# Optimization experiments

Measured on AMD Instinct MI355X. Metric: run time of the kernel, lower is better.

The kernel has to match this reference:

```python
import jax, jax.numpy as jnp
import numpy as np

B, M, NH, EH = 16, 128, 256, 128


def setup_inputs() -> dict:
    key = jax.random.key(0)
    ks = jax.random.split(key, 10)
    s = 0.05
    return {
        "X": jax.random.normal(ks[0], (B, M, NH), dtype=jnp.float32),
        "E": jax.random.normal(ks[1], (B, M, M, EH), dtype=jnp.float32),
        "A": jax.random.uniform(ks[2], (B, M, M), dtype=jnp.float32),
        "w": jax.random.uniform(ks[3], (B, M, 1), dtype=jnp.float32),
        "Wv_w": jax.random.normal(ks[4], (NH, NH), dtype=jnp.float32) * s,
        "Wv_b": jnp.zeros((NH,), dtype=jnp.float32),
        "We_w": jax.random.normal(ks[5], (EH, EH), dtype=jnp.float32) * s,
        "We_b": jnp.zeros((EH,), dtype=jnp.float32),
        "Wu_w": jax.random.normal(ks[6], (2 * NH + EH, NH), dtype=jnp.float32) * s,
        "Wu_b": jnp.zeros((NH,), dtype=jnp.float32),
    }


def reference(X, E, A, w, Wv_w, Wv_b, We_w, We_b, Wu_w, Wu_b):
    act = jax.nn.relu
    # W_v / W_e single-layer FFNs (capacity=0 -> one Linear)
    node_map = X @ Wv_w + Wv_b                      # [B, m, nh]
    edge_map = E @ We_w + We_b                      # [B, m, m, eh]
    # Fused aggregation: sum_i A[b,i,j] * cat(node_map[b,i], edge_map[b,i,j])
    # (avoids materializing the [B,m,m,nh+eh] intermediate; same math)
    agg_node = jnp.einsum('bij,bid->bjd', A, node_map)   # [B, m, nh]
    agg_edge = jnp.einsum('bij,bije->bje', A, edge_map)  # [B, m, eh]
    h = jnp.concatenate([agg_node, agg_edge, X], axis=2) # [B, m, 2nh+eh]
    out = (act(h) @ Wu_w + Wu_b) * w                     # [B, m, nh]
    return out
```

## Files before the change

### kernel.cpp

```cpp
#include <hip/hip_runtime.h>

namespace {

constexpr int Bn   = 16;
constexpr int Mn   = 128;
constexpr int NHn  = 256;
constexpr int EHn  = 128;
constexpr int ROWS = Bn * Mn;
constexpr int HW   = 2 * NHn + EHn;

constexpr int HP = HW + 4;
constexpr int AP = NHn + 4;
constexpr int TP = EHn + 4;

__device__ __forceinline__ float4 f4zero() { return make_float4(0.f, 0.f, 0.f, 0.f); }
__device__ __forceinline__ float4 ld4(const float* p) {
    return *reinterpret_cast<const float4*>(p);
}
__device__ __forceinline__ void f4fma(float4& acc, float a, const float4& v) {
    acc.x = fmaf(a, v.x, acc.x);
    acc.y = fmaf(a, v.y, acc.y);
    acc.z = fmaf(a, v.z, acc.z);
    acc.w = fmaf(a, v.w, acc.w);
}
__device__ __forceinline__ float4 f4add(const float4& a, const float4& b) {
    return make_float4(a.x + b.x, a.y + b.y, a.z + b.z, a.w + b.w);
}
__device__ __forceinline__ float4 f4relu(const float4& a) {
    return make_float4(fmaxf(a.x, 0.f), fmaxf(a.y, 0.f),
                       fmaxf(a.z, 0.f), fmaxf(a.w, 0.f));
}

#define LOADW(B, wb, ldw, kk) {                                        \
    const float* _wp = (wb) + (size_t)(kk) * (ldw);                    \
    B[0] = ld4(_wp);                 B[1] = ld4(_wp + (ldw));          \
    B[2] = ld4(_wp + 2 * (ldw));     B[3] = ld4(_wp + 3 * (ldw)); }

#define FMA2R(B, kk, opA, opB) {                                       \
    const float4 _ha = ld4(&(opA)[kk]);                                \
    const float4 _hb = ld4(&(opB)[kk]);                                \
    f4fma(a0, _ha.x, B[0]); f4fma(a1, _hb.x, B[0]);                    \
    f4fma(a0, _ha.y, B[1]); f4fma(a1, _hb.y, B[1]);                    \
    f4fma(a0, _ha.z, B[2]); f4fma(a1, _hb.z, B[2]);                    \
    f4fma(a0, _ha.w, B[3]); f4fma(a1, _hb.w, B[3]); }

#define FMA1R(B, kk, opA) {                                            \
    const float4 _ha = ld4(&(opA)[kk]);                                \
    f4fma(a0, _ha.x, B[0]); f4fma(a0, _ha.y, B[1]);                    \
    f4fma(a0, _ha.z, B[2]); f4fma(a0, _ha.w, B[3]); }

__global__ __launch_bounds__(256) void k_reduce(
    const float* __restrict__ E, const float* __restrict__ A,
    float* __restrict__ T)
{
    const int bid = blockIdx.x;
    const int b   = bid >> 5;
    const int j0  = (bid & 31) * 4;
    const int tid = threadIdx.x;

    __shared__ float acolT[4][Mn];

    if (tid < Mn) {
        const float4 a4 = ld4(A + (size_t)b * Mn * Mn + (size_t)tid * Mn + j0);
        acolT[0][tid] = a4.x; acolT[1][tid] = a4.y;
        acolT[2][tid] = a4.z; acolT[3][tid] = a4.w;
    }
    __syncthreads();

    const int jj = tid >> 6;
    const int f2 = tid & 63;
    const float* Eb = E + (size_t)b * Mn * Mn * EHn + (size_t)(j0 + jj) * EHn
                        + f2 * 2;
    const float* ac = acolT[jj];

    float2 acc = make_float2(0.f, 0.f);
    #pragma unroll 16
    for (int i = 0; i < Mn; ++i) {
        const float2 e2 = *reinterpret_cast<const float2*>(
            Eb + (size_t)i * (Mn * EHn));
        const float a = ac[i];
        acc.x = fmaf(a, e2.x, acc.x);
        acc.y = fmaf(a, e2.y, acc.y);
    }

    const int row = b * Mn + j0 + jj;
    *reinterpret_cast<float2*>(T + (size_t)row * EHn + f2 * 2) = acc;
}

__global__ __launch_bounds__(512, 2) void k_mix(
    const float* __restrict__ T, const float* __restrict__ A,
    const float* __restrict__ X,
    const float* __restrict__ Wv, const float* __restrict__ Wvb,
    const float* __restrict__ We, const float* __restrict__ Web,
    const float* __restrict__ Wu, const float* __restrict__ Wub,
    const float* __restrict__ wrow, float* __restrict__ out)
{
    const int r0  = blockIdx.x * 8;
    const int b   = r0 >> 7;
    const int j0  = r0 & 127;
    const int tid = threadIdx.x;

    __shared__ float  asl[Mn][8];
    __shared__ float  ts[8][TP];
    __shared__ float  axs[8][AP];
    __shared__ float  hs[8][HP];
    __shared__ float4 comb[256][2];
    __shared__ float  pcs[8][8];
    __shared__ float  csb[8];

    {
        const int i = tid >> 2, q = tid & 3;
        const float2 a2 = *reinterpret_cast<const float2*>(
            A + (size_t)b * Mn * Mn + (size_t)i * Mn + j0 + q * 2);
        asl[i][q * 2]     = a2.x;
        asl[i][q * 2 + 1] = a2.y;
    }
    if (tid < 256) {
        const int r = tid >> 5, c = tid & 31;
        *reinterpret_cast<float4*>(&ts[r][c * 4]) =
            ld4(T + (size_t)(r0 + r) * EHn + c * 4);
    }
    {
        const int r = tid >> 6, c4 = tid & 63;
        const float4 x4 = ld4(X + (size_t)(r0 + r) * NHn + c4 * 4);
        *reinterpret_cast<float4*>(&hs[r][NHn + EHn + c4 * 4]) = f4relu(x4);
    }
    __syncthreads();

    const int t8 = tid & 255;
    const int rg = t8 >> 6;
    const int c4 = t8 & 63;
    const int kh = tid >> 8;
    const int ra = 2 * rg, rb = ra + 1;

    if (tid < 64) {
        const int r = tid >> 3, seg = tid & 7;
        float s = 0.f;
        #pragma unroll
        for (int i = 0; i < 16; ++i) s += asl[seg * 16 + i][r];
        pcs[r][seg] = s;
    }

    {
        const float* wb = X + (size_t)(b * Mn) * NHn + c4 * 4;
        const int k0 = kh * 64;
        float4 B0[4], B1[4];
        float4 a0 = f4zero(), a1 = f4zero();
        LOADW(B0, wb, NHn, k0);
        for (int k = k0; k < k0 + 64; k += 8) {
            LOADW(B1, wb, NHn, k + 4);
            {
                const float4 _b = B0[0];
                (void)_b;
            }
            {
                f4fma(a0, asl[k    ][ra], B0[0]); f4fma(a1, asl[k    ][rb], B0[0]);
                f4fma(a0, asl[k + 1][ra], B0[1]); f4fma(a1, asl[k + 1][rb], B0[1]);
                f4fma(a0, asl[k + 2][ra], B0[2]); f4fma(a1, asl[k + 2][rb], B0[2]);
                f4fma(a0, asl[k + 3][ra], B0[3]); f4fma(a1, asl[k + 3][rb], B0[3]);
            }
            if (k + 8 < k0 + 64) LOADW(B0, wb, NHn, k + 8);
            {
                f4fma(a0, asl[k + 4][ra], B1[0]); f4fma(a1, asl[k + 4][rb], B1[0]);
                f4fma(a0, asl[k + 5][ra], B1[1]); f4fma(a1, asl[k + 5][rb], B1[1]);
                f4fma(a0, asl[k + 6][ra], B1[2]); f4fma(a1, asl[k + 6][rb], B1[2]);
                f4fma(a0, asl[k + 7][ra], B1[3]); f4fma(a1, asl[k + 7][rb], B1[3]);
            }
        }
        if (kh == 1) { comb[t8][0] = a0; comb[t8][1] = a1; }
        __syncthreads();
        if (kh == 0) {
            a0 = f4add(a0, comb[t8][0]);
            a1 = f4add(a1, comb[t8][1]);
            *reinterpret_cast<float4*>(&axs[ra][c4 * 4]) = a0;
            *reinterpret_cast<float4*>(&axs[rb][c4 * 4]) = a1;
        }
        if (tid < 8) {
            float s = 0.f;
            #pragma unroll
            for (int g = 0; g < 8; ++g) s += pcs[tid][g];
            csb[tid] = s;
        }
        __syncthreads();
    }

    if (tid < 256) {
        const int er = tid >> 5;
        const int ec = tid & 31;
        const float* wb = We + ec * 4;
        const float* opA = ts[er];
        float4 B0[4], B1[4];
        float4 a0 = f4zero();
        LOADW(B0, wb, EHn, 0);
        for (int k = 0; k < EHn; k += 8) {
            LOADW(B1, wb, EHn, k + 4);
            FMA1R(B0, k, opA);
            if (k + 8 < EHn) LOADW(B0, wb, EHn, k + 8);
            FMA1R(B1, k + 4, opA);
        }
        const float4 be = ld4(Web + ec * 4);
        f4fma(a0, csb[er], be);
        *reinterpret_cast<float4*>(&hs[er][NHn + ec * 4]) = f4relu(a0);
    }

    {
        const float* wb = Wv + c4 * 4;
        const float* opA = axs[ra];
        const float* opB = axs[rb];
        const int k0 = kh * 128;
        float4 B0[4], B1[4];
        float4 a0 = f4zero(), a1 = f4zero();
        LOADW(B0, wb, NHn, k0);
        for (int k = k0; k < k0 + 128; k += 8) {
            LOADW(B1, wb, NHn, k + 4);
            FMA2R(B0, k, opA, opB);
            if (k + 8 < k0 + 128) LOADW(B0, wb, NHn, k + 8);
            FMA2R(B1, k + 4, opA, opB);
        }
        if (kh == 1) { comb[t8][0] = a0; comb[t8][1] = a1; }
        __syncthreads();
        if (kh == 0) {
            a0 = f4add(a0, comb[t8][0]);
            a1 = f4add(a1, comb[t8][1]);
            const float4 bv = ld4(Wvb + c4 * 4);
            f4fma(a0, csb[ra], bv);
            f4fma(a1, csb[rb], bv);
            *reinterpret_cast<float4*>(&hs[ra][c4 * 4]) = f4relu(a0);
            *reinterpret_cast<float4*>(&hs[rb][c4 * 4]) = f4relu(a1);
        }
        __syncthreads();
    }

    {
        const float* wb = Wu + c4 * 4;
        const float* opA = hs[ra];
        const float* opB = hs[rb];
        const int k0 = kh * 320;
        float4 B0[4], B1[4];
        float4 a0 = f4zero(), a1 = f4zero();
        LOADW(B0, wb, NHn, k0);
        for (int k = k0; k < k0 + 320; k += 8) {
            LOADW(B1, wb, NHn, k + 4);
            FMA2R(B0, k, opA, opB);
            if (k + 8 < k0 + 320) LOADW(B0, wb, NHn, k + 8);
            FMA2R(B1, k + 4, opA, opB);
        }
        if (kh == 1) { comb[t8][0] = a0; comb[t8][1] = a1; }
        __syncthreads();
        if (kh == 0) {
            a0 = f4add(a0, comb[t8][0]);
            a1 = f4add(a1, comb[t8][1]);
            const float4 bu = ld4(Wub + c4 * 4);
            const float w0 = wrow[r0 + ra], w1 = wrow[r0 + rb];
            float4 o0, o1;
            o0.x = (a0.x + bu.x) * w0;  o0.y = (a0.y + bu.y) * w0;
            o0.z = (a0.z + bu.z) * w0;  o0.w = (a0.w + bu.w) * w0;
            o1.x = (a1.x + bu.x) * w1;  o1.y = (a1.y + bu.y) * w1;
            o1.z = (a1.z + bu.z) * w1;  o1.w = (a1.w + bu.w) * w1;
            *reinterpret_cast<float4*>(out + (size_t)(r0 + ra) * NHn + c4 * 4) = o0;
            *reinterpret_cast<float4*>(out + (size_t)(r0 + rb) * NHn + c4 * 4) = o1;
        }
    }
}

}

extern "C" void kernel_launch(void* const* d_in, const int* in_sizes, int n_in,
                              void* d_out, int out_size, void* d_ws, size_t ws_size,
                              hipStream_t stream) {
    const float* X   = (const float*)d_in[0];
    const float* E   = (const float*)d_in[1];
    const float* A   = (const float*)d_in[2];
    const float* w   = (const float*)d_in[3];
    const float* Wv  = (const float*)d_in[4];
    const float* Wvb = (const float*)d_in[5];
    const float* We  = (const float*)d_in[6];
    const float* Web = (const float*)d_in[7];
    const float* Wu  = (const float*)d_in[8];
    const float* Wub = (const float*)d_in[9];
    float* out = (float*)d_out;

    float* T = (float*)d_ws;

    k_reduce<<<512, 256, 0, stream>>>(E, A, T);
    k_mix<<<256, 512, 0, stream>>>(T, A, X, Wv, Wvb, We, Web, Wu, Wub, w, out);
}
```

Baseline: 260.3 us.

## Restructure mix kernel to four rows per block with per-column threads

Rewrites the mix kernel so each 256-thread block handles 4 output rows, with each thread computing one output column across all four rows. Scalar FMAs replace the float4 register tiling and split-K combine. The intent is to double the block count for better occupancy and fewer synchronisations. In exchange, weights are reused across fewer rows, which roughly doubles the weight reads from cache.

```diff
diff --git a/kernel.cpp b/kernel.cpp
--- a/kernel.cpp
+++ b/kernel.cpp
@@ -9,45 +9,13 @@
 constexpr int ROWS = Bn * Mn;
 constexpr int HW   = 2 * NHn + EHn;
 
-constexpr int HP = HW + 4;
-constexpr int AP = NHn + 4;
-constexpr int TP = EHn + 4;
-
-__device__ __forceinline__ float4 f4zero() { return make_float4(0.f, 0.f, 0.f, 0.f); }
 __device__ __forceinline__ float4 ld4(const float* p) {
     return *reinterpret_cast<const float4*>(p);
-}
-__device__ __forceinline__ void f4fma(float4& acc, float a, const float4& v) {
-    acc.x = fmaf(a, v.x, acc.x);
-    acc.y = fmaf(a, v.y, acc.y);
-    acc.z = fmaf(a, v.z, acc.z);
-    acc.w = fmaf(a, v.w, acc.w);
-}
-__device__ __forceinline__ float4 f4add(const float4& a, const float4& b) {
-    return make_float4(a.x + b.x, a.y + b.y, a.z + b.z, a.w + b.w);
 }
 __device__ __forceinline__ float4 f4relu(const float4& a) {
     return make_float4(fmaxf(a.x, 0.f), fmaxf(a.y, 0.f),
                        fmaxf(a.z, 0.f), fmaxf(a.w, 0.f));
 }
-
-#define LOADW(B, wb, ldw, kk) {                                        \
-    const float* _wp = (wb) + (size_t)(kk) * (ldw);                    \
-    B[0] = ld4(_wp);                 B[1] = ld4(_wp + (ldw));          \
-    B[2] = ld4(_wp + 2 * (ldw));     B[3] = ld4(_wp + 3 * (ldw)); }
-
-#define FMA2R(B, kk, opA, opB) {                                       \
-    const float4 _ha = ld4(&(opA)[kk]);                                \
-    const float4 _hb = ld4(&(opB)[kk]);                                \
-    f4fma(a0, _ha.x, B[0]); f4fma(a1, _hb.x, B[0]);                    \
-    f4fma(a0, _ha.y, B[1]); f4fma(a1, _hb.y, B[1]);                    \
-    f4fma(a0, _ha.z, B[2]); f4fma(a1, _hb.z, B[2]);                    \
-    f4fma(a0, _ha.w, B[3]); f4fma(a1, _hb.w, B[3]); }
-
-#define FMA1R(B, kk, opA) {                                            \
-    const float4 _ha = ld4(&(opA)[kk]);                                \
-    f4fma(a0, _ha.x, B[0]); f4fma(a0, _ha.y, B[1]);                    \
-    f4fma(a0, _ha.z, B[2]); f4fma(a0, _ha.w, B[3]); }
 
 __global__ __launch_bounds__(256) void k_reduce(
     const float* __restrict__ E, const float* __restrict__ A,
@@ -87,7 +55,7 @@
     *reinterpret_cast<float2*>(T + (size_t)row * EHn + f2 * 2) = acc;
 }
 
-__global__ __launch_bounds__(512, 2) void k_mix(
+__global__ __launch_bounds__(256) void k_mix(
     const float* __restrict__ T, const float* __restrict__ A,
     const float* __restrict__ X,
     const float* __restrict__ Wv, const float* __restrict__ Wvb,
@@ -95,171 +63,145 @@
     const float* __restrict__ Wu, const float* __restrict__ Wub,
     const float* __restrict__ wrow, float* __restrict__ out)
 {
-    const int r0  = blockIdx.x * 8;
-    const int b   = r0 >> 7;
-    const int j0  = r0 & 127;
+    const int bid = blockIdx.x;
+    const int b   = bid >> 5;
+    const int j0  = (bid & 31) * 4;
+    const int r0  = b * Mn + j0;
     const int tid = threadIdx.x;
 
-    __shared__ float  asl[Mn][8];
-    __shared__ float  ts[8][TP];
-    __shared__ float  axs[8][AP];
-    __shared__ float  hs[8][HP];
-    __shared__ float4 comb[256][2];
-    __shared__ float  pcs[8][8];
-    __shared__ float  csb[8];
-
-    {
-        const int i = tid >> 2, q = tid & 3;
-        const float2 a2 = *reinterpret_cast<const float2*>(
-            A + (size_t)b * Mn * Mn + (size_t)i * Mn + j0 + q * 2);
-        asl[i][q * 2]     = a2.x;
-        asl[i][q * 2 + 1] = a2.y;
-    }
-    if (tid < 256) {
-        const int r = tid >> 5, c = tid & 31;
+    __shared__ float acolT[4][Mn];
+    __shared__ float ts[4][EHn];
+    __shared__ float axs[4][NHn];
+    __shared__ float hs[4][HW];
+    __shared__ float pec[2][4][EHn];
+    __shared__ float pcs[4][16];
+    __shared__ float csb[4];
+
+    if (tid < Mn) {
+        const float4 a4 = ld4(A + (size_t)b * Mn * Mn + (size_t)tid * Mn + j0);
+        acolT[0][tid] = a4.x; acolT[1][tid] = a4.y;
+        acolT[2][tid] = a4.z; acolT[3][tid] = a4.w;
+    } else {
+        const int t = tid - 128;
+        const int r = t >> 5, c = t & 31;
         *reinterpret_cast<float4*>(&ts[r][c * 4]) =
             ld4(T + (size_t)(r0 + r) * EHn + c * 4);
     }
     {
-        const int r = tid >> 6, c4 = tid & 63;
-        const float4 x4 = ld4(X + (size_t)(r0 + r) * NHn + c4 * 4);
-        *reinterpret_cast<float4*>(&hs[r][NHn + EHn + c4 * 4]) = f4relu(x4);
-    }
-    __syncthreads();
-
-    const int t8 = tid & 255;
-    const int rg = t8 >> 6;
-    const int c4 = t8 & 63;
-    const int kh = tid >> 8;
-    const int ra = 2 * rg, rb = ra + 1;
+        const int r = tid >> 6, c = tid & 63;
+        const float4 x4 = ld4(X + (size_t)(r0 + r) * NHn + c * 4);
+        *reinterpret_cast<float4*>(&hs[r][NHn + EHn + c * 4]) = f4relu(x4);
+    }
+    __syncthreads();
 
     if (tid < 64) {
-        const int r = tid >> 3, seg = tid & 7;
-        float s = 0.f;
+        const int r = tid >> 4, s = tid & 15;
+        float acc = 0.f;
         #pragma unroll
-        for (int i = 0; i < 16; ++i) s += asl[seg * 16 + i][r];
-        pcs[r][seg] = s;
-    }
-
-    {
-        const float* wb = X + (size_t)(b * Mn) * NHn + c4 * 4;
+        for (int i = 0; i < 8; ++i) acc += acolT[r][s * 8 + i];
+        pcs[r][s] = acc;
+    }
+    if (tid < 4) {
+        float acc = 0.f;
+        #pragma unroll
+        for (int s = 0; s < 16; ++s) acc += pcs[tid][s];
+        csb[tid] = acc;
+    }
+
+    {
+        const float* Xb = X + (size_t)(b * Mn) * NHn + tid;
+        float a0 = 0.f, a1 = 0.f, a2 = 0.f, a3 = 0.f;
+        for (int k = 0; k < Mn; k += 16) {
+            float xw[16];
+            #pragma unroll
+            for (int u = 0; u < 16; ++u) xw[u] = Xb[(size_t)(k + u) * NHn];
+            #pragma unroll
+            for (int u = 0; u < 16; ++u) {
+                a0 = fmaf(acolT[0][k + u], xw[u], a0);
+                a1 = fmaf(acolT[1][k + u], xw[u], a1);
+                a2 = fmaf(acolT[2][k + u], xw[u], a2);
+                a3 = fmaf(acolT[3][k + u], xw[u], a3);
+            }
+        }
+        axs[0][tid] = a0; axs[1][tid] = a1;
+        axs[2][tid] = a2; axs[3][tid] = a3;
+    }
+    __syncthreads();
+
+    {
+        const float* Wvc = Wv + tid;
+        float n0 = 0.f, n1 = 0.f, n2 = 0.f, n3 = 0.f;
+        for (int k = 0; k < NHn; k += 16) {
+            float wv[16];
+            #pragma unroll
+            for (int u = 0; u < 16; ++u) wv[u] = Wvc[(size_t)(k + u) * NHn];
+            #pragma unroll
+            for (int u = 0; u < 16; ++u) {
+                n0 = fmaf(axs[0][k + u], wv[u], n0);
+                n1 = fmaf(axs[1][k + u], wv[u], n1);
+                n2 = fmaf(axs[2][k + u], wv[u], n2);
+                n3 = fmaf(axs[3][k + u], wv[u], n3);
+            }
+        }
+        const float bv = Wvb[tid];
+        hs[0][tid] = fmaxf(fmaf(csb[0], bv, n0), 0.f);
+        hs[1][tid] = fmaxf(fmaf(csb[1], bv, n1), 0.f);
+        hs[2][tid] = fmaxf(fmaf(csb[2], bv, n2), 0.f);
+        hs[3][tid] = fmaxf(fmaf(csb[3], bv, n3), 0.f);
+    }
+
+    {
+        const int kh = tid >> 7;
+        const int c  = tid & 127;
         const int k0 = kh * 64;
-        float4 B0[4], B1[4];
-        float4 a0 = f4zero(), a1 = f4zero();
-        LOADW(B0, wb, NHn, k0);
-        for (int k = k0; k < k0 + 64; k += 8) {
-            LOADW(B1, wb, NHn, k + 4);
-            {
-                const float4 _b = B0[0];
-                (void)_b;
-            }
-            {
-                f4fma(a0, asl[k    ][ra], B0[0]); f4fma(a1, asl[k    ][rb], B0[0]);
-                f4fma(a0, asl[k + 1][ra], B0[1]); f4fma(a1, asl[k + 1][rb], B0[1]);
-                f4fma(a0, asl[k + 2][ra], B0[2]); f4fma(a1, asl[k + 2][rb], B0[2]);
-                f4fma(a0, asl[k + 3][ra], B0[3]); f4fma(a1, asl[k + 3][rb], B0[3]);
-            }
-            if (k + 8 < k0 + 64) LOADW(B0, wb, NHn, k + 8);
-            {
-                f4fma(a0, asl[k + 4][ra], B1[0]); f4fma(a1, asl[k + 4][rb], B1[0]);
-                f4fma(a0, asl[k + 5][ra], B1[1]); f4fma(a1, asl[k + 5][rb], B1[1]);
-                f4fma(a0, asl[k + 6][ra], B1[2]); f4fma(a1, asl[k + 6][rb], B1[2]);
-                f4fma(a0, asl[k + 7][ra], B1[3]); f4fma(a1, asl[k + 7][rb], B1[3]);
-            }
-        }
-        if (kh == 1) { comb[t8][0] = a0; comb[t8][1] = a1; }
-        __syncthreads();
-        if (kh == 0) {
-            a0 = f4add(a0, comb[t8][0]);
-            a1 = f4add(a1, comb[t8][1]);
-            *reinterpret_cast<float4*>(&axs[ra][c4 * 4]) = a0;
-            *reinterpret_cast<float4*>(&axs[rb][c4 * 4]) = a1;
-        }
-        if (tid < 8) {
-            float s = 0.f;
-            #pragma unroll
-            for (int g = 0; g < 8; ++g) s += pcs[tid][g];
-            csb[tid] = s;
-        }
-        __syncthreads();
-    }
-
-    if (tid < 256) {
-        const int er = tid >> 5;
-        const int ec = tid & 31;
-        const float* wb = We + ec * 4;
-        const float* opA = ts[er];
-        float4 B0[4], B1[4];
-        float4 a0 = f4zero();
-        LOADW(B0, wb, EHn, 0);
-        for (int k = 0; k < EHn; k += 8) {
-            LOADW(B1, wb, EHn, k + 4);
-            FMA1R(B0, k, opA);
-            if (k + 8 < EHn) LOADW(B0, wb, EHn, k + 8);
-            FMA1R(B1, k + 4, opA);
-        }
-        const float4 be = ld4(Web + ec * 4);
-        f4fma(a0, csb[er], be);
-        *reinterpret_cast<float4*>(&hs[er][NHn + ec * 4]) = f4relu(a0);
-    }
-
-    {
-        const float* wb = Wv + c4 * 4;
-        const float* opA = axs[ra];
-        const float* opB = axs[rb];
-        const int k0 = kh * 128;
-        float4 B0[4], B1[4];
-        float4 a0 = f4zero(), a1 = f4zero();
-        LOADW(B0, wb, NHn, k0);
-        for (int k = k0; k < k0 + 128; k += 8) {
-            LOADW(B1, wb, NHn, k + 4);
-            FMA2R(B0, k, opA, opB);
-            if (k + 8 < k0 + 128) LOADW(B0, wb, NHn, k + 8);
-            FMA2R(B1, k + 4, opA, opB);
-        }
-        if (kh == 1) { comb[t8][0] = a0; comb[t8][1] = a1; }
-        __syncthreads();
-        if (kh == 0) {
-            a0 = f4add(a0, comb[t8][0]);
-            a1 = f4add(a1, comb[t8][1]);
-            const float4 bv = ld4(Wvb + c4 * 4);
-            f4fma(a0, csb[ra], bv);
-            f4fma(a1, csb[rb], bv);
-            *reinterpret_cast<float4*>(&hs[ra][c4 * 4]) = f4relu(a0);
-            *reinterpret_cast<float4*>(&hs[rb][c4 * 4]) = f4relu(a1);
-        }
-        __syncthreads();
-    }
-
-    {
-        const float* wb = Wu + c4 * 4;
-        const float* opA = hs[ra];
-        const float* opB = hs[rb];
-        const int k0 = kh * 320;
-        float4 B0[4], B1[4];
-        float4 a0 = f4zero(), a1 = f4zero();
-        LOADW(B0, wb, NHn, k0);
-        for (int k = k0; k < k0 + 320; k += 8) {
-            LOADW(B1, wb, NHn, k + 4);
-            FMA2R(B0, k, opA, opB);
-            if (k + 8 < k0 + 320) LOADW(B0, wb, NHn, k + 8);
-            FMA2R(B1, k + 4, opA, opB);
-        }
-        if (kh == 1) { comb[t8][0] = a0; comb[t8][1] = a1; }
-        __syncthreads();
-        if (kh == 0) {
-            a0 = f4add(a0, comb[t8][0]);
-            a1 = f4add(a1, comb[t8][1]);
-            const float4 bu = ld4(Wub + c4 * 4);
-            const float w0 = wrow[r0 + ra], w1 = wrow[r0 + rb];
-            float4 o0, o1;
-            o0.x = (a0.x + bu.x) * w0;  o0.y = (a0.y + bu.y) * w0;
-            o0.z = (a0.z + bu.z) * w0;  o0.w = (a0.w + bu.w) * w0;
-            o1.x = (a1.x + bu.x) * w1;  o1.y = (a1.y + bu.y) * w1;
-            o1.z = (a1.z + bu.z) * w1;  o1.w = (a1.w + bu.w) * w1;
-            *reinterpret_cast<float4*>(out + (size_t)(r0 + ra) * NHn + c4 * 4) = o0;
-            *reinterpret_cast<float4*>(out + (size_t)(r0 + rb) * NHn + c4 * 4) = o1;
-        }
+        const float* Wec = We + c;
+        float e0 = 0.f, e1 = 0.f, e2 = 0.f, e3 = 0.f;
+        for (int k = k0; k < k0 + 64; k += 16) {
+            float we[16];
+            #pragma unroll
+            for (int u = 0; u < 16; ++u) we[u] = Wec[(size_t)(k + u) * EHn];
+            #pragma unroll
+            for (int u = 0; u < 16; ++u) {
+                e0 = fmaf(ts[0][k + u], we[u], e0);
+                e1 = fmaf(ts[1][k + u], we[u], e1);
+                e2 = fmaf(ts[2][k + u], we[u], e2);
+                e3 = fmaf(ts[3][k + u], we[u], e3);
+            }
+        }
+        pec[kh][0][c] = e0; pec[kh][1][c] = e1;
+        pec[kh][2][c] = e2; pec[kh][3][c] = e3;
+    }
+    __syncthreads();
+    if (tid < 128) {
+        const float be = Web[tid];
+        #pragma unroll
+        for (int r = 0; r < 4; ++r) {
+            const float e = pec[0][r][tid] + pec[1][r][tid];
+            hs[r][NHn + tid] = fmaxf(fmaf(csb[r], be, e), 0.f);
+        }
+    }
+    __syncthreads();
+
+    {
+        const float* Wuc = Wu + tid;
+        float o0 = 0.f, o1 = 0.f, o2 = 0.f, o3 = 0.f;
+        for (int k = 0; k < HW; k += 16) {
+            float wu[16];
+            #pragma unroll
+            for (int u = 0; u < 16; ++u) wu[u] = Wuc[(size_t)(k + u) * NHn];
+            #pragma unroll
+            for (int u = 0; u < 16; ++u) {
+                o0 = fmaf(hs[0][k + u], wu[u], o0);
+                o1 = fmaf(hs[1][k + u], wu[u], o1);
+                o2 = fmaf(hs[2][k + u], wu[u], o2);
+                o3 = fmaf(hs[3][k + u], wu[u], o3);
+            }
+        }
+        const float bu = Wub[tid];
+        out[(size_t)(r0 + 0) * NHn + tid] = (o0 + bu) * wrow[r0 + 0];
+        out[(size_t)(r0 + 1) * NHn + tid] = (o1 + bu) * wrow[r0 + 1];
+        out[(size_t)(r0 + 2) * NHn + tid] = (o2 + bu) * wrow[r0 + 2];
+        out[(size_t)(r0 + 3) * NHn + tid] = (o3 + bu) * wrow[r0 + 3];
     }
 }
 
@@ -283,5 +225,5 @@
     float* T = (float*)d_ws;
 
     k_reduce<<<512, 256, 0, stream>>>(E, A, T);
-    k_mix<<<256, 512, 0, stream>>>(T, A, X, Wv, Wvb, We, Web, Wu, Wub, w, out);
-}
+    k_mix<<<512, 256, 0, stream>>>(T, A, X, Wv, Wvb, We, Web, Wu, Wub, w, out);
+}
```

Result: no change. 258.8 us (-0.6%).
